# Optimization experiments

Measured on AMD Instinct MI355X. Metric: run time of the kernel, lower is better.

Reference implementation:

```python
import jax, jax.numpy as jnp
import numpy as np
from jax import lax

# Quantization params from symmetric_linear_quantization_params(num_bits=5, sat=9):
# n = 2**(5-1)-1 = 15, scale = 15/9, zero_point = 0
Q_SCALE = 15.0 / 9.0
Q_ZP = 0.0


def ste_quant_dequant(y, scale=Q_SCALE, zp=Q_ZP):
    # forward: round(scale*y - zp); dequant: (q + zp)/scale. backward: identity (STE).
    q = jnp.round(scale * y - zp)
    dq = (q + zp) / scale
    return y + lax.stop_gradient(dq - y)


def setup_inputs() -> dict:
    key = jax.random.key(0)
    k1, k2, k3 = jax.random.split(key, 3)
    B, Cin, H, Wd = 8, 16, 112, 112
    Cout, KH, KW = 32, 3, 3
    x = jax.random.normal(k1, (B, Cin, H, Wd), dtype=jnp.float32)
    # per-input-channel conv weights: [Cin, Cout, 1, KH, KW]
    W = jax.random.normal(k2, (Cin, Cout, 1, KH, KW), dtype=jnp.float32) * (1.0 / np.sqrt(KH * KW))
    b = jax.random.normal(k3, (Cin, Cout), dtype=jnp.float32) * 0.1
    return {"x": x, "W": W, "b": b}


def reference(x, W, b):
    B, Cin, H, Wd = x.shape
    Cout = W.shape[1]
    # Fuse the in_channels separate 1->Cout convs into one grouped conv:
    # weight [Cin*Cout, 1, KH, KW], feature_group_count=Cin
    w_grouped = W.reshape(Cin * Cout, 1, W.shape[3], W.shape[4])
    y = lax.conv_general_dilated(
        x, w_grouped,
        window_strides=(1, 1),
        padding=((1, 1), (1, 1)),
        dimension_numbers=("NCHW", "OIHW", "NCHW"),
        feature_group_count=Cin,
    )  # [B, Cin*Cout, H, W]
    y = y.reshape(B, Cin, Cout, y.shape[2], y.shape[3])
    y = y + b[None, :, :, None, None]
    # quantize-dequant each per-input-channel partial output, then sum over Cin
    out = jnp.sum(ste_quant_dequant(y), axis=1)  # [B, Cout, H, W]
    return out
```

## Files before the change

kernel.cpp:

```cpp
#include <hip/hip_runtime.h>


typedef float v2f __attribute__((ext_vector_type(2)));

constexpr int B_    = 8;
constexpr int CIN   = 16;
constexpr int COUT  = 32;
constexpr int H_    = 112;
constexpr int W_    = 112;
constexpr int TW    = 16;
constexpr int TH    = 8;
constexpr int HW_   = TW + 2;
constexpr int HH_   = TH + 2;
constexpr int LDSW  = 20;
constexpr int COG   = 8;

__global__ __launch_bounds__(256, 4)
void conv_quant_sum_kernel(const float* __restrict__ x,
                           const float* __restrict__ w,
                           const float* __restrict__ bias,
                           float* __restrict__ out)
{
#pragma clang fp contract(off)
    const float QS = (float)(15.0 / 9.0);
    const float DQ = 0.6f;

    __shared__ float xs[CIN][HH_][LDSW];

    const int t    = threadIdx.x;
    const int lane = t & 63;
    const int tx   = lane & 7;
    const int ty   = lane >> 3;
    const int wid  = __builtin_amdgcn_readfirstlane(t >> 6);
    const int cog  = wid * COG;

    const int tile_x = blockIdx.x * TW;
    const int tile_y = blockIdx.y * TH;
    const int b      = blockIdx.z;

    const float* xb = x + (size_t)b * CIN * H_ * W_;
    for (int idx = t; idx < CIN * HH_ * HW_; idx += 256) {
        int ci  = idx / (HH_ * HW_);
        int rem = idx - ci * (HH_ * HW_);
        int r   = rem / HW_;
        int c   = rem - r * HW_;
        int gh  = tile_y + r - 1;
        int gw  = tile_x + c - 1;
        float v = 0.0f;
        if ((unsigned)gh < (unsigned)H_ && (unsigned)gw < (unsigned)W_)
            v = xb[ci * H_ * W_ + gh * W_ + gw];
        xs[ci][r][c] = v;
    }
    __syncthreads();

    v2f acc[COG];
#pragma unroll
    for (int co = 0; co < COG; ++co) acc[co] = v2f{0.0f, 0.0f};

    for (int ci = 0; ci < CIN; ++ci) {
        v2f xw[3][3];
#pragma unroll
        for (int r = 0; r < 3; ++r) {
            const float* row = &xs[ci][ty + r][2 * tx];
            v2f p0 = *reinterpret_cast<const v2f*>(row);
            v2f p1 = *reinterpret_cast<const v2f*>(row + 2);
            xw[r][0] = p0;
            xw[r][1] = v2f{p0.y, p1.x};
            xw[r][2] = p1;
        }

        const float* wc = w + (ci * COUT + cog) * 9;
        const float* bc = bias + ci * COUT + cog;
#pragma unroll
        for (int co = 0; co < COG; ++co) {
            v2f s = v2f{0.0f, 0.0f};
#pragma unroll
            for (int k = 0; k < 9; ++k) {
                float wv = wc[co * 9 + k];
                s = __builtin_elementwise_fma(xw[k / 3][k % 3], v2f{wv, wv}, s);
            }
            float bv = bc[co];
            v2f y  = s + v2f{bv, bv};
            v2f tq = y * v2f{QS, QS};
            v2f q;
            q.x = rintf(tq.x);
            q.y = rintf(tq.y);
            acc[co] = __builtin_elementwise_fma(q, v2f{DQ, DQ}, acc[co]);
        }
    }

    float* ob = out + ((size_t)b * COUT + cog) * H_ * W_;
    const int oh = tile_y + ty;
    const int ow = tile_x + 2 * tx;
#pragma unroll
    for (int co = 0; co < COG; ++co)
        *reinterpret_cast<v2f*>(ob + co * H_ * W_ + oh * W_ + ow) = acc[co];
}

extern "C" void kernel_launch(void* const* d_in, const int* in_sizes, int n_in,
                              void* d_out, int out_size, void* d_ws, size_t ws_size,
                              hipStream_t stream)
{
    const float* x    = (const float*)d_in[0];
    const float* w    = (const float*)d_in[1];
    const float* bias = (const float*)d_in[2];
    float* out        = (float*)d_out;

    dim3 grid(W_ / TW, H_ / TH, B_);
    dim3 block(256);
    conv_quant_sum_kernel<<<grid, block, 0, stream>>>(x, w, bias, out);
}
```

Measured before the change: 83.31 us.

## Split output channels across two blocks and batch halo loads per thread

Doubles the grid by giving each block half of the output channels, so each wave computes 4 channels instead of 8. This gives more blocks and lower per-thread register pressure. The halo tile load now has each thread fetch one spatial position for all 16 input channels, with the loads issued up front instead of through an index-division loop. Each input tile is now loaded twice, by two blocks, which adds redundant global and LDS traffic. Columns 18-19 of the LDS row are now written with padding values; they sit outside the read window.

```diff
diff --git a/kernel.cpp b/kernel.cpp
--- a/kernel.cpp
+++ b/kernel.cpp
@@ -10,10 +10,9 @@
 constexpr int W_    = 112;
 constexpr int TW    = 16;
 constexpr int TH    = 8;
-constexpr int HW_   = TW + 2;
+constexpr int LDSW  = 20;
 constexpr int HH_   = TH + 2;
-constexpr int LDSW  = 20;
-constexpr int COG   = 8;
+constexpr int COG   = 4;
 
 __global__ __launch_bounds__(256, 4)
 void conv_quant_sum_kernel(const float* __restrict__ x,
@@ -32,24 +31,34 @@
     const int tx   = lane & 7;
     const int ty   = lane >> 3;
     const int wid  = __builtin_amdgcn_readfirstlane(t >> 6);
-    const int cog  = wid * COG;
 
     const int tile_x = blockIdx.x * TW;
     const int tile_y = blockIdx.y * TH;
-    const int b      = blockIdx.z;
+    const int b      = blockIdx.z >> 1;
+    const int cog    = (blockIdx.z & 1) * 16 + wid * COG;
 
     const float* xb = x + (size_t)b * CIN * H_ * W_;
-    for (int idx = t; idx < CIN * HH_ * HW_; idx += 256) {
-        int ci  = idx / (HH_ * HW_);
-        int rem = idx - ci * (HH_ * HW_);
-        int r   = rem / HW_;
-        int c   = rem - r * HW_;
-        int gh  = tile_y + r - 1;
-        int gw  = tile_x + c - 1;
-        float v = 0.0f;
-        if ((unsigned)gh < (unsigned)H_ && (unsigned)gw < (unsigned)W_)
-            v = xb[ci * H_ * W_ + gh * W_ + gw];
-        xs[ci][r][c] = v;
+    {
+        const int sr = t / 20;
+        const int sc = t - sr * 20;
+        const bool active = (sr < HH_);
+        const int gh = tile_y + sr - 1;
+        const int gw = tile_x + sc - 1;
+        const bool inb = active && ((unsigned)gh < (unsigned)H_) &&
+                         ((unsigned)gw < (unsigned)W_);
+        const float* sp = inb ? (xb + gh * W_ + gw) : xb;
+        float v[CIN];
+#pragma unroll
+        for (int ci = 0; ci < CIN; ++ci)
+            v[ci] = sp[ci * (H_ * W_)];
+#pragma unroll
+        for (int ci = 0; ci < CIN; ++ci)
+            v[ci] = inb ? v[ci] : 0.0f;
+        if (active) {
+#pragma unroll
+            for (int ci = 0; ci < CIN; ++ci)
+                xs[ci][sr][sc] = v[ci];
+        }
     }
     __syncthreads();
 
@@ -106,7 +115,7 @@
     const float* bias = (const float*)d_in[2];
     float* out        = (float*)d_out;
 
-    dim3 grid(W_ / TW, H_ / TH, B_);
+    dim3 grid(W_ / TW, H_ / TH, B_ * 2);
     dim3 block(256);
     conv_quant_sum_kernel<<<grid, block, 0, stream>>>(x, w, bias, out);
 }
```

New measurement: 83.95 us. Within noise of the previous version (+0.8%).
